# Optimization experiments

Hardware: AMD Instinct MI355X
Metric: run time of the kernel (lower is better)

## Reference

```python
import jax, jax.numpy as jnp
import numpy as np

B, T, E, H = 32, 256, 512, 512


def setup_inputs() -> dict:
    key = jax.random.key(0)
    ks = jax.random.split(key, 9)
    s_e = 1.0 / np.sqrt(E)  # nn.Linear default init bound
    s_h = 1.0 / np.sqrt(H)

    def u(k, shape, s):
        return jax.random.uniform(k, shape, jnp.float32, -s, s)

    # Gate order along the 4H axis: [in, forget, cell, out]
    return {
        "x": jax.random.normal(ks[0], (B, T, E), jnp.float32),
        "fwd_Wih": u(ks[1], (E, 4 * H), s_e),
        "fwd_bih": u(ks[2], (4 * H,), s_e),
        "fwd_Whh": u(ks[3], (H, 4 * H), s_h),
        "fwd_bhh": u(ks[4], (4 * H,), s_h),
        "bwd_Wih": u(ks[5], (E, 4 * H), s_e),
        "bwd_bih": u(ks[6], (4 * H,), s_e),
        "bwd_Whh": u(ks[7], (H, 4 * H), s_h),
        "bwd_bhh": u(ks[8], (4 * H,), s_h),
    }


def _lstm(x_seq, Wih, bih, Whh, bhh):
    """Run one LSTM direction over x_seq [B,T,E]; returns hidden states [B,T,H]
    in scan order (no flipping), matching the torch loop."""
    b, h = x_seq.shape[0], Whh.shape[0]
    # Precompute all input projections (and fold both biases) in one big GEMM.
    xg = jnp.einsum("bte,eg->tbg", x_seq, Wih) + bih + bhh  # [T,B,4H]
    h0 = jnp.zeros((b, h), x_seq.dtype)
    c0 = jnp.zeros((b, h), x_seq.dtype)

    def step(carry, xg_t):
        hprev, cprev = carry
        g = xg_t + hprev @ Whh  # [B,4H]
        i, f, gc, o = jnp.split(g, 4, axis=-1)
        c = jax.nn.sigmoid(f) * cprev + jax.nn.sigmoid(i) * jnp.tanh(gc)
        hnew = jax.nn.sigmoid(o) * jnp.tanh(c)
        return (hnew, c), hnew

    _, hs = jax.lax.scan(step, (h0, c0), xg)  # hs: [T,B,H]
    return hs.transpose(1, 0, 2)


def reference(x, fwd_Wih, fwd_bih, fwd_Whh, fwd_bhh,
              bwd_Wih, bwd_bih, bwd_Whh, bwd_bhh):
    fwd = _lstm(x, fwd_Wih, fwd_bih, fwd_Whh, fwd_bhh)
    # Backward direction processes reversed inputs; outputs are stacked in
    # processing order (the torch module does NOT re-flip them).
    bwd = _lstm(x[:, ::-1, :], bwd_Wih, bwd_bih, bwd_Whh, bwd_bhh)
    return jnp.concatenate([fwd, bwd], axis=-1)  # [B,T,2H]
```

## Files before the change

kernel.cpp:

```cpp
#include <hip/hip_runtime.h>
#include <hip/hip_bf16.h>
#include <math.h>

static constexpr int BB = 32;
static constexpr int TT = 256;
static constexpr int EE = 512;
static constexpr int HH = 512;
static constexpr int GG = 2048;

static constexpr int WS = 20;
static constexpr int HS = 36;

using u16 = unsigned short;

__device__ __forceinline__ float bf2f(u16 u) {
    return __uint_as_float(((unsigned int)u) << 16);
}
__device__ __forceinline__ u16 f2bf(float f) {
    unsigned int u = __float_as_uint(f);
    unsigned int r = 0x7FFFu + ((u >> 16) & 1u);
    return (u16)((u + r) >> 16);
}
__device__ __forceinline__ float sigm(float x) {
    return 1.0f / (1.0f + expf(-x));
}

__device__ __forceinline__ float4 ld_b128_sc(const float4* p) {
    float4 v;
    asm volatile("global_load_dwordx4 %0, %1, off sc0 sc1" : "=v"(v) : "v"(p));
    return v;
}
__device__ __forceinline__ void st_b32_sc(float* p, float v) {
    asm volatile("global_store_dword %0, %1, off sc0 sc1" :: "v"(p), "v"(v) : "memory");
}

template<bool F32>
__device__ __forceinline__ float ldw(const void* p, size_t i) {
    if constexpr (F32) return ((const float*)p)[i];
    else               return bf2f(((const u16*)p)[i]);
}
template<bool F32>
__device__ __forceinline__ float4 ld4(const void* p, size_t i) {
    if constexpr (F32) {
        return *(const float4*)((const float*)p + i);
    } else {
        ushort4 v = *(const ushort4*)((const u16*)p + i);
        return make_float4(bf2f(v.x), bf2f(v.y), bf2f(v.z), bf2f(v.w));
    }
}

__global__ void init_state(const u16* __restrict__ bih_probe,
                           float* __restrict__ h_st, float* __restrict__ c_st,
                           int* __restrict__ bar, int* __restrict__ flag) {
    size_t i = (size_t)blockIdx.x * blockDim.x + threadIdx.x;
    size_t stride = (size_t)gridDim.x * blockDim.x;
    for (size_t j = i; j < (size_t)2*2*BB*HH; j += stride) h_st[j] = 0.0f;
    for (size_t j = i; j < (size_t)2*BB*HH;   j += stride) c_st[j] = 0.0f;
    for (size_t j = i; j < 1024;              j += stride) bar[j] = 0;
    if (blockIdx.x == 0 && threadIdx.x == 0) {
        int f = 0;
        for (int k = 0; k < 2048; ++k) {
            int e = (bih_probe[k] >> 7) & 0xFF;
            if (e >= 127) f = 1;
        }
        *flag = f;
    }
}

template<bool F32>
__device__ __forceinline__ void xg_body(
    const void* __restrict__ x, const void* __restrict__ Wih,
    const void* __restrict__ bih, const void* __restrict__ bhh,
    float* __restrict__ xgp, int d, int mt, int nt, float* b_lds)
{
    const int tid = threadIdx.x;
    const int tn = tid & 15;
    const int tm = tid >> 4;
    const int m0 = mt * 64;
    const int n0 = nt * 64;

    size_t a_off[4];
    #pragma unroll
    for (int i = 0; i < 4; ++i) {
        const int m = m0 + 4*tm + i;
        const int t = m >> 5, b = m & 31;
        const int t_src = d ? (TT - 1 - t) : t;
        a_off[i] = ((size_t)b * TT + t_src) * EE;
    }

    float acc[4][4];
    #pragma unroll
    for (int i = 0; i < 4; ++i)
        #pragma unroll
        for (int j = 0; j < 4; ++j) acc[i][j] = 0.0f;

    const int kr = tid >> 2;
    const int nc = (tid & 3) * 16;

    for (int k0 = 0; k0 < EE; k0 += 64) {
        __syncthreads();
        #pragma unroll 4
        for (int e = 0; e < 16; ++e)
            b_lds[kr*64 + nc + e] = ldw<F32>(Wih, (size_t)(k0 + kr)*GG + n0 + nc + e);
        __syncthreads();

        #pragma unroll 2
        for (int kk = 0; kk < 64; kk += 4) {
            float4 av[4];
            #pragma unroll
            for (int i = 0; i < 4; ++i) av[i] = ld4<F32>(x, a_off[i] + k0 + kk);
            #pragma unroll
            for (int j = 0; j < 4; ++j) {
                const float4 bv = *(const float4*)&b_lds[(kk + j)*64 + 4*tn];
                #pragma unroll
                for (int i = 0; i < 4; ++i) {
                    const float a = (j == 0) ? av[i].x : (j == 1) ? av[i].y
                                  : (j == 2) ? av[i].z : av[i].w;
                    acc[i][0] += a * bv.x; acc[i][1] += a * bv.y;
                    acc[i][2] += a * bv.z; acc[i][3] += a * bv.w;
                }
            }
        }
    }

    const int mbase = m0 + 4*tm;
    const int tt = mbase >> 5, bb = mbase & 31;
    #pragma unroll
    for (int j = 0; j < 4; ++j) {
        const int col  = n0 + 4*tn + j;
        const float bs = ldw<F32>(bih, col) + ldw<F32>(bhh, col);
        const int g    = col >> 9;
        const int nblk = (col & 511) >> 2;
        const int nl   = col & 3;
        const size_t idx = (((size_t)d*TT + tt)*65536)
                         + (size_t)nblk*512 + (size_t)(g*4 + nl)*32 + bb;
        float4 v = make_float4(acc[0][j] + bs, acc[1][j] + bs,
                               acc[2][j] + bs, acc[3][j] + bs);
        *(float4*)&xgp[idx] = v;
    }
}

__global__ __launch_bounds__(256) void xg_gemm(
    const void* __restrict__ x,
    const void* __restrict__ WihF, const void* __restrict__ bihF, const void* __restrict__ bhhF,
    const void* __restrict__ WihB, const void* __restrict__ bihB, const void* __restrict__ bhhB,
    float* __restrict__ xgp, const int* __restrict__ flag)
{
    __shared__ float b_lds[64 * 64];
    const int bid = blockIdx.x;
    const int d  = bid >> 12;
    const int r  = bid & 4095;
    const int mt = r >> 5;
    const int nt = r & 31;
    const void* Wih = d ? WihB : WihF;
    const void* bih = d ? bihB : bihF;
    const void* bhh = d ? bhhB : bhhF;
    if (*flag) xg_body<true >(x, Wih, bih, bhh, xgp, d, mt, nt, b_lds);
    else       xg_body<false>(x, Wih, bih, bhh, xgp, d, mt, nt, b_lds);
}

__device__ __forceinline__ void grid_bar_dir(int* __restrict__ bard, int wgl, int target) {
    asm volatile("s_waitcnt vmcnt(0)" ::: "memory");
    __syncthreads();
    if (threadIdx.x == 0) {
        int v = __hip_atomic_fetch_add(&bard[32 + (wgl >> 4) * 32], 1,
                                       __ATOMIC_RELAXED, __HIP_MEMORY_SCOPE_AGENT);
        if ((v & 15) == 15)
            __hip_atomic_fetch_add(&bard[0], 1, __ATOMIC_RELAXED, __HIP_MEMORY_SCOPE_AGENT);
        while (__hip_atomic_load(&bard[0], __ATOMIC_RELAXED, __HIP_MEMORY_SCOPE_AGENT) < target)
            __builtin_amdgcn_s_sleep(1);
    }
    __syncthreads();
}

template<bool F32>
__device__ __forceinline__ void rec_body(
    const void* __restrict__ Whh,
    const float* __restrict__ xgp,
    float* __restrict__ hT,
    int* __restrict__ bar,
    void* __restrict__ out, int d, int nblk, int wgl,
    float* __restrict__ wT_lds,
    float* __restrict__ h_lds,
    float* __restrict__ gbuf)
{
    const int tid = threadIdx.x;
    const int cg = tid >> 6;
    const int bg = (tid >> 3) & 7;
    const int kg = tid & 7;

    {
        const int ci = tid & 15;
        const int cw = (ci >> 2)*512 + nblk*4 + (ci & 3);
        const int kb = (tid >> 4) * 32;
        #pragma unroll 4
        for (int k = kb; k < kb + 32; ++k)
            wT_lds[k*WS + ci] = ldw<F32>(Whh, (size_t)k*GG + cw);
    }

    int* bard = bar + d*512;
    float cr = 0.0f;
    const int gnl = tid >> 5;
    const int gb  = tid & 31;

    __syncthreads();

    for (int t = 0; t < TT; ++t) {
        const int parity = t & 1;
        const float4* hprev4 = (const float4*)(hT + (size_t)(d*2 + (parity ^ 1)) * 16384);
        float*        hnext  = hT + (size_t)(d*2 + parity) * 16384;

        float xgv[4] = {0.f, 0.f, 0.f, 0.f};
        if (tid < 128) {
            const float* xgs = xgp + (((size_t)d*TT + t)*65536) + (size_t)nblk*512;
            #pragma unroll
            for (int g = 0; g < 4; ++g)
                xgv[g] = xgs[(g*4 + gnl)*32 + gb];
        }

        float4 hstg[16];
        #pragma unroll
        for (int i = 0; i < 16; ++i)
            hstg[i] = ld_b128_sc(hprev4 + i*256 + tid);
        asm volatile("s_waitcnt vmcnt(0)" ::: "memory");
        __builtin_amdgcn_sched_barrier(0);
        #pragma unroll
        for (int i = 0; i < 16; ++i) {
            const int idx = i*256 + tid;
            const int k  = idx >> 3;
            const int b4 = idx & 7;
            *(float4*)&h_lds[k*HS + b4*4] = hstg[i];
        }
        __syncthreads();

        float acc[4][4];
        #pragma unroll
        for (int i = 0; i < 4; ++i)
            #pragma unroll
            for (int j = 0; j < 4; ++j) acc[i][j] = 0.0f;
        {
            const float* wp = wT_lds + kg*WS + cg*4;
            const float* hp = h_lds  + kg*HS + bg*4;
            #pragma unroll 8
            for (int kk = 0; kk < 64; ++kk) {
                const float4 wv = *(const float4*)(wp + kk*(8*WS));
                const float4 hv = *(const float4*)(hp + kk*(8*HS));
                acc[0][0] += wv.x*hv.x; acc[0][1] += wv.x*hv.y; acc[0][2] += wv.x*hv.z; acc[0][3] += wv.x*hv.w;
                acc[1][0] += wv.y*hv.x; acc[1][1] += wv.y*hv.y; acc[1][2] += wv.y*hv.z; acc[1][3] += wv.y*hv.w;
                acc[2][0] += wv.z*hv.x; acc[2][1] += wv.z*hv.y; acc[2][2] += wv.z*hv.z; acc[2][3] += wv.z*hv.w;
                acc[3][0] += wv.w*hv.x; acc[3][1] += wv.w*hv.y; acc[3][2] += wv.w*hv.z; acc[3][3] += wv.w*hv.w;
            }
        }
        #pragma unroll
        for (int i = 0; i < 4; ++i)
            #pragma unroll
            for (int j = 0; j < 4; ++j) {
                float v = acc[i][j];
                v += __shfl_xor(v, 1);
                v += __shfl_xor(v, 2);
                v += __shfl_xor(v, 4);
                acc[i][j] = v;
            }
        if (kg < 4) {
            const int ci = kg;
            *(float4*)&gbuf[(cg*4 + ci)*32 + bg*4] =
                make_float4(acc[ci][0], acc[ci][1], acc[ci][2], acc[ci][3]);
        }
        __syncthreads();

        if (tid < 128) {
            const int nl = gnl;
            const int b  = gb;
            const float gi = gbuf[(0*4 + nl)*32 + b] + xgv[0];
            const float gf = gbuf[(1*4 + nl)*32 + b] + xgv[1];
            const float gc = gbuf[(2*4 + nl)*32 + b] + xgv[2];
            const float go = gbuf[(3*4 + nl)*32 + b] + xgv[3];
            const float cn = sigm(gf)*cr + sigm(gi)*tanhf(gc);
            cr = cn;
            const float hv = sigm(go)*tanhf(cn);
            const int ng = nblk*4 + nl;
            st_b32_sc(hnext + (size_t)ng*32 + b, hv);
            const size_t oi = ((size_t)b*TT + t)*(2*HH) + (size_t)d*HH + ng;
            if constexpr (F32) ((float*)out)[oi] = hv;
            else               ((u16*)out)[oi]   = f2bf(hv);
        }
        grid_bar_dir(bard, wgl, 8 * (t + 1));
    }
}

__global__ __launch_bounds__(256, 1) void lstm_rec(
    const void* __restrict__ WhhF, const void* __restrict__ WhhB,
    const float* __restrict__ xgp, float* __restrict__ hT,
    int* __restrict__ bar, const int* __restrict__ flag,
    void* __restrict__ out)
{
    __shared__ float wT_lds[512 * WS];
    __shared__ float h_lds[512 * HS];
    __shared__ float gbuf[512];
    const int wg   = blockIdx.x;
    const int d    = wg >> 7;
    const int nblk = wg & 127;
    const void* Whh = d ? WhhB : WhhF;
    if (*flag) rec_body<true >(Whh, xgp, hT, bar, out, d, nblk, wg & 127, wT_lds, h_lds, gbuf);
    else       rec_body<false>(Whh, xgp, hT, bar, out, d, nblk, wg & 127, wT_lds, h_lds, gbuf);
}

template<bool F32>
__device__ __forceinline__ void step_body(
    const void* __restrict__ x,
    const void* __restrict__ Wih, const void* __restrict__ bih,
    const void* __restrict__ Whh, const void* __restrict__ bhh,
    const float* __restrict__ h_prev, float* __restrict__ h_next,
    float* __restrict__ c_st, void* __restrict__ out,
    int d, int nblk, int t, int t_src, float* __restrict__ gbuf)
{
    const int tid = threadIdx.x;
    const int c0  = tid & 15;
    const int g   = c0 >> 2;
    const int nl  = c0 & 3;
    const int bq  = tid >> 4;
    const int col = g*512 + nblk*4 + nl;
    const int b0 = bq*2, b1 = b0 + 1;

    float p00=0.f,p01=0.f,p02=0.f,p03=0.f;
    float p10=0.f,p11=0.f,p12=0.f,p13=0.f;
    {
        const size_t xo0 = ((size_t)b0*TT + t_src) * EE;
        const size_t xo1 = ((size_t)b1*TT + t_src) * EE;
        #pragma unroll 4
        for (int k = 0; k < EE; k += 4) {
            const size_t wi = (size_t)k*GG + col;
            float w0 = ldw<F32>(Wih, wi);
            float w1 = ldw<F32>(Wih, wi +   (size_t)GG);
            float w2 = ldw<F32>(Wih, wi + 2*(size_t)GG);
            float w3 = ldw<F32>(Wih, wi + 3*(size_t)GG);
            float4 a0 = ld4<F32>(x, xo0 + k);
            float4 a1 = ld4<F32>(x, xo1 + k);
            p00 += w0*a0.x; p01 += w1*a0.y; p02 += w2*a0.z; p03 += w3*a0.w;
            p10 += w0*a1.x; p11 += w1*a1.y; p12 += w2*a1.z; p13 += w3*a1.w;
        }
    }
    {
        const float* hr0 = h_prev + (size_t)b0*HH;
        const float* hr1 = h_prev + (size_t)b1*HH;
        #pragma unroll 4
        for (int k = 0; k < HH; k += 4) {
            const size_t wi = (size_t)k*GG + col;
            float w0 = ldw<F32>(Whh, wi);
            float w1 = ldw<F32>(Whh, wi +   (size_t)GG);
            float w2 = ldw<F32>(Whh, wi + 2*(size_t)GG);
            float w3 = ldw<F32>(Whh, wi + 3*(size_t)GG);
            float4 v0 = *(const float4*)(hr0 + k);
            float4 v1 = *(const float4*)(hr1 + k);
            p00 += w0*v0.x; p01 += w1*v0.y; p02 += w2*v0.z; p03 += w3*v0.w;
            p10 += w0*v1.x; p11 += w1*v1.y; p12 += w2*v1.z; p13 += w3*v1.w;
        }
    }
    const float bias = ldw<F32>(bih, col) + ldw<F32>(bhh, col);
    gbuf[tid*2 + 0] = p00 + p01 + p02 + p03 + bias;
    gbuf[tid*2 + 1] = p10 + p11 + p12 + p13 + bias;
    __syncthreads();
    if (c0 < 4) {
        const int nlc = c0;
        const int ng  = nblk*4 + nlc;
        #pragma unroll
        for (int bi = 0; bi < 2; ++bi) {
            const int b = bq*2 + bi;
            const float gi = gbuf[(bq*16 + 0  + nlc)*2 + bi];
            const float gf = gbuf[(bq*16 + 4  + nlc)*2 + bi];
            const float gc = gbuf[(bq*16 + 8  + nlc)*2 + bi];
            const float go = gbuf[(bq*16 + 12 + nlc)*2 + bi];
            const size_t ci = (size_t)b*HH + ng;
            const float cp = c_st[ci];
            const float cn = sigm(gf)*cp + sigm(gi)*tanhf(gc);
            c_st[ci] = cn;
            const float hv = sigm(go)*tanhf(cn);
            h_next[ci] = hv;
            const size_t oi = ((size_t)b*TT + t)*(2*HH) + (size_t)d*HH + ng;
            if constexpr (F32) ((float*)out)[oi] = hv;
            else               ((u16*)out)[oi]   = f2bf(hv);
        }
    }
}

__global__ __launch_bounds__(256) void lstm_step(
    const void* __restrict__ x,
    const void* __restrict__ WihF, const void* __restrict__ bihF,
    const void* __restrict__ WhhF, const void* __restrict__ bhhF,
    const void* __restrict__ WihB, const void* __restrict__ bihB,
    const void* __restrict__ WhhB, const void* __restrict__ bhhB,
    float* __restrict__ h_buf, float* __restrict__ c_buf,
    const int* __restrict__ flag, void* __restrict__ out, int t)
{
    __shared__ float gbuf[512];
    const int bid  = blockIdx.x;
    const int d    = bid >> 7;
    const int nblk = bid & 127;
    const void* Wih = d ? WihB : WihF;
    const void* Whh = d ? WhhB : WhhF;
    const void* bih = d ? bihB : bihF;
    const void* bhh = d ? bhhB : bhhF;
    const int t_src  = d ? (TT - 1 - t) : t;
    const int parity = t & 1;
    const float* h_prev = h_buf + ((size_t)(d*2 + (parity ^ 1))) * BB * HH;
    float*       h_next = h_buf + ((size_t)(d*2 + parity)) * BB * HH;
    float*       c_st   = c_buf + (size_t)d * BB * HH;
    if (*flag) step_body<true >(x, Wih, bih, Whh, bhh, h_prev, h_next, c_st, out, d, nblk, t, t_src, gbuf);
    else       step_body<false>(x, Wih, bih, Whh, bhh, h_prev, h_next, c_st, out, d, nblk, t, t_src, gbuf);
}

extern "C" void kernel_launch(void* const* d_in, const int* in_sizes, int n_in,
                              void* d_out, int out_size, void* d_ws, size_t ws_size,
                              hipStream_t stream) {
    const void* x    = d_in[0];
    const void* WihF = d_in[1];
    const void* bihF = d_in[2];
    const void* WhhF = d_in[3];
    const void* bhhF = d_in[4];
    const void* WihB = d_in[5];
    const void* bihB = d_in[6];
    const void* WhhB = d_in[7];
    const void* bhhB = d_in[8];

    float* ws = (float*)d_ws;

    const size_t off_xg = 0;
    const size_t off_h  = (size_t)2*TT*BB*GG;
    const size_t off_c  = off_h + (size_t)2*2*BB*HH;
    const size_t off_b  = off_c + (size_t)2*BB*HH;
    const size_t off_f  = off_b + 1024;
    const size_t need_bytes = (off_f + 16) * sizeof(float);

    if (ws_size >= need_bytes) {
        float* xgp  = ws + off_xg;
        float* hT   = ws + off_h;
        float* cbuf = ws + off_c;
        int*   bar  = (int*)(ws + off_b);
        int*   flag = (int*)(ws + off_f);

        init_state<<<64, 256, 0, stream>>>((const u16*)bihF, hT, cbuf, bar, flag);
        xg_gemm<<<8192, 256, 0, stream>>>(x, WihF, bihF, bhhF, WihB, bihB, bhhB, xgp, flag);
        lstm_rec<<<256, 256, 0, stream>>>(WhhF, WhhB, xgp, hT, bar, flag, d_out);
    } else {
        float* h_buf = ws;
        float* c_buf = ws + (size_t)2*2*BB*HH;
        int*   bar   = (int*)(c_buf + (size_t)2*BB*HH);
        int*   flag  = (int*)(bar + 1024);
        init_state<<<64, 256, 0, stream>>>((const u16*)bihF, h_buf, c_buf, bar, flag);
        for (int t = 0; t < TT; ++t) {
            lstm_step<<<256, 256, 0, stream>>>(x, WihF, bihF, WhhF, bhhF,
                                               WihB, bihB, WhhB, bhhB,
                                               h_buf, c_buf, flag, d_out, t);
        }
    }
}
```

Baseline: 2.629 ms.

## Replace two-level grid barrier with split arrive/wait and chunked h staging

```diff
diff --git a/kernel.cpp b/kernel.cpp
--- a/kernel.cpp
+++ b/kernel.cpp
@@ -32,6 +32,19 @@
 }
 __device__ __forceinline__ void st_b32_sc(float* p, float v) {
     asm volatile("global_store_dword %0, %1, off sc0 sc1" :: "v"(p), "v"(v) : "memory");
+}
+
+__device__ __forceinline__ void waitcnt_chunk(int g) {
+    switch (g) {
+    case 0: asm volatile("s_waitcnt vmcnt(14)" ::: "memory"); break;
+    case 1: asm volatile("s_waitcnt vmcnt(12)" ::: "memory"); break;
+    case 2: asm volatile("s_waitcnt vmcnt(10)" ::: "memory"); break;
+    case 3: asm volatile("s_waitcnt vmcnt(8)"  ::: "memory"); break;
+    case 4: asm volatile("s_waitcnt vmcnt(6)"  ::: "memory"); break;
+    case 5: asm volatile("s_waitcnt vmcnt(4)"  ::: "memory"); break;
+    case 6: asm volatile("s_waitcnt vmcnt(2)"  ::: "memory"); break;
+    default: asm volatile("s_waitcnt vmcnt(0)" ::: "memory"); break;
+    }
 }
 
 template<bool F32>
@@ -159,20 +172,6 @@
     else       xg_body<false>(x, Wih, bih, bhh, xgp, d, mt, nt, b_lds);
 }
 
-__device__ __forceinline__ void grid_bar_dir(int* __restrict__ bard, int wgl, int target) {
-    asm volatile("s_waitcnt vmcnt(0)" ::: "memory");
-    __syncthreads();
-    if (threadIdx.x == 0) {
-        int v = __hip_atomic_fetch_add(&bard[32 + (wgl >> 4) * 32], 1,
-                                       __ATOMIC_RELAXED, __HIP_MEMORY_SCOPE_AGENT);
-        if ((v & 15) == 15)
-            __hip_atomic_fetch_add(&bard[0], 1, __ATOMIC_RELAXED, __HIP_MEMORY_SCOPE_AGENT);
-        while (__hip_atomic_load(&bard[0], __ATOMIC_RELAXED, __HIP_MEMORY_SCOPE_AGENT) < target)
-            __builtin_amdgcn_s_sleep(1);
-    }
-    __syncthreads();
-}
-
 template<bool F32>
 __device__ __forceinline__ void rec_body(
     const void* __restrict__ Whh,
@@ -184,7 +183,8 @@
     float* __restrict__ h_lds,
     float* __restrict__ gbuf)
 {
-    const int tid = threadIdx.x;
+    const int tid  = threadIdx.x;
+    const int lane = tid & 63;
     const int cg = tid >> 6;
     const int bg = (tid >> 3) & 7;
     const int kg = tid & 7;
@@ -199,9 +199,14 @@
     }
 
     int* bard = bar + d*512;
+    int* grpc = bard + 32;
+    const int mygrp = wgl >> 4;
     float cr = 0.0f;
     const int gnl = tid >> 5;
     const int gb  = tid & 31;
+
+    const float* wp = wT_lds + kg*WS + cg*4;
+    const float* hp = h_lds  + kg*HS + bg*4;
 
     __syncthreads();
 
@@ -218,31 +223,44 @@
                 xgv[g] = xgs[(g*4 + gnl)*32 + gb];
         }
 
+        if (t > 0) {
+            const int tgt = 16 * t;
+            while (true) {
+                int v = 0x7fffffff;
+                if (lane < 8)
+                    v = __hip_atomic_load(&grpc[lane*32], __ATOMIC_RELAXED,
+                                          __HIP_MEMORY_SCOPE_AGENT);
+                if (__all(v >= tgt)) break;
+                __builtin_amdgcn_s_sleep(1);
+            }
+        }
+        __builtin_amdgcn_sched_barrier(0);
+
         float4 hstg[16];
         #pragma unroll
         for (int i = 0; i < 16; ++i)
             hstg[i] = ld_b128_sc(hprev4 + i*256 + tid);
-        asm volatile("s_waitcnt vmcnt(0)" ::: "memory");
-        __builtin_amdgcn_sched_barrier(0);
-        #pragma unroll
-        for (int i = 0; i < 16; ++i) {
-            const int idx = i*256 + tid;
-            const int k  = idx >> 3;
-            const int b4 = idx & 7;
-            *(float4*)&h_lds[k*HS + b4*4] = hstg[i];
-        }
-        __syncthreads();
 
         float acc[4][4];
         #pragma unroll
         for (int i = 0; i < 4; ++i)
             #pragma unroll
             for (int j = 0; j < 4; ++j) acc[i][j] = 0.0f;
-        {
-            const float* wp = wT_lds + kg*WS + cg*4;
-            const float* hp = h_lds  + kg*HS + bg*4;
-            #pragma unroll 8
-            for (int kk = 0; kk < 64; ++kk) {
+
+        #pragma unroll
+        for (int g2 = 0; g2 < 8; ++g2) {
+            waitcnt_chunk(g2);
+            #pragma unroll
+            for (int j = 0; j < 2; ++j) {
+                const int idx = (2*g2 + j)*256 + tid;
+                const int k  = idx >> 3;
+                const int b4 = idx & 7;
+                *(float4*)&h_lds[k*HS + b4*4] = hstg[2*g2 + j];
+            }
+            asm volatile("s_waitcnt lgkmcnt(0)\n\ts_barrier" ::: "memory");
+            #pragma unroll
+            for (int kkl = 0; kkl < 8; ++kkl) {
+                const int kk = g2*8 + kkl;
                 const float4 wv = *(const float4*)(wp + kk*(8*WS));
                 const float4 hv = *(const float4*)(hp + kk*(8*HS));
                 acc[0][0] += wv.x*hv.x; acc[0][1] += wv.x*hv.y; acc[0][2] += wv.x*hv.z; acc[0][3] += wv.x*hv.w;
@@ -251,6 +269,7 @@
                 acc[3][0] += wv.w*hv.x; acc[3][1] += wv.w*hv.y; acc[3][2] += wv.w*hv.z; acc[3][3] += wv.w*hv.w;
             }
         }
+
         #pragma unroll
         for (int i = 0; i < 4; ++i)
             #pragma unroll
@@ -284,7 +303,12 @@
             if constexpr (F32) ((float*)out)[oi] = hv;
             else               ((u16*)out)[oi]   = f2bf(hv);
         }
-        grid_bar_dir(bard, wgl, 8 * (t + 1));
+
+        asm volatile("s_waitcnt vmcnt(0)" ::: "memory");
+        __syncthreads();
+        if (tid == 0)
+            __hip_atomic_fetch_add(&grpc[mygrp*32], 1,
+                                   __ATOMIC_RELAXED, __HIP_MEMORY_SCOPE_AGENT);
     }
 }
 
```

Result: slower. 2.852 ms (+8.5%).

## Replace two-level grid barrier with per-group counters and prefetch next-step gate inputs

Applied to the files above, without the earlier changes.

```diff
diff --git a/kernel.cpp b/kernel.cpp
--- a/kernel.cpp
+++ b/kernel.cpp
@@ -25,11 +25,6 @@
     return 1.0f / (1.0f + expf(-x));
 }
 
-__device__ __forceinline__ float4 ld_b128_sc(const float4* p) {
-    float4 v;
-    asm volatile("global_load_dwordx4 %0, %1, off sc0 sc1" : "=v"(v) : "v"(p));
-    return v;
-}
 __device__ __forceinline__ void st_b32_sc(float* p, float v) {
     asm volatile("global_store_dword %0, %1, off sc0 sc1" :: "v"(p), "v"(v) : "memory");
 }
@@ -159,20 +154,6 @@
     else       xg_body<false>(x, Wih, bih, bhh, xgp, d, mt, nt, b_lds);
 }
 
-__device__ __forceinline__ void grid_bar_dir(int* __restrict__ bard, int wgl, int target) {
-    asm volatile("s_waitcnt vmcnt(0)" ::: "memory");
-    __syncthreads();
-    if (threadIdx.x == 0) {
-        int v = __hip_atomic_fetch_add(&bard[32 + (wgl >> 4) * 32], 1,
-                                       __ATOMIC_RELAXED, __HIP_MEMORY_SCOPE_AGENT);
-        if ((v & 15) == 15)
-            __hip_atomic_fetch_add(&bard[0], 1, __ATOMIC_RELAXED, __HIP_MEMORY_SCOPE_AGENT);
-        while (__hip_atomic_load(&bard[0], __ATOMIC_RELAXED, __HIP_MEMORY_SCOPE_AGENT) < target)
-            __builtin_amdgcn_s_sleep(1);
-    }
-    __syncthreads();
-}
-
 template<bool F32>
 __device__ __forceinline__ void rec_body(
     const void* __restrict__ Whh,
@@ -184,7 +165,8 @@
     float* __restrict__ h_lds,
     float* __restrict__ gbuf)
 {
-    const int tid = threadIdx.x;
+    const int tid  = threadIdx.x;
+    const int lane = tid & 63;
     const int cg = tid >> 6;
     const int bg = (tid >> 3) & 7;
     const int kg = tid & 7;
@@ -199,31 +181,51 @@
     }
 
     int* bard = bar + d*512;
+    int* grpc = bard + 32;
+    const int mygrp = wgl >> 4;
     float cr = 0.0f;
     const int gnl = tid >> 5;
     const int gb  = tid & 31;
 
+    const float* wp = wT_lds + kg*WS + cg*4;
+    const float* hp = h_lds  + kg*HS + bg*4;
+
     __syncthreads();
+
+    float xgv[4] = {0.f, 0.f, 0.f, 0.f};
+    if (tid < 128) {
+        const float* xgs = xgp + ((size_t)d*TT)*65536 + (size_t)nblk*512;
+        #pragma unroll
+        for (int g = 0; g < 4; ++g)
+            xgv[g] = xgs[(g*4 + gnl)*32 + gb];
+    }
 
     for (int t = 0; t < TT; ++t) {
         const int parity = t & 1;
         const float4* hprev4 = (const float4*)(hT + (size_t)(d*2 + (parity ^ 1)) * 16384);
         float*        hnext  = hT + (size_t)(d*2 + parity) * 16384;
 
-        float xgv[4] = {0.f, 0.f, 0.f, 0.f};
-        if (tid < 128) {
-            const float* xgs = xgp + (((size_t)d*TT + t)*65536) + (size_t)nblk*512;
-            #pragma unroll
-            for (int g = 0; g < 4; ++g)
-                xgv[g] = xgs[(g*4 + gnl)*32 + gb];
-        }
+        if (tid < 64) {
+            if (t > 0) {
+                const int tgt = 16 * t;
+                while (true) {
+                    int v = 0x7fffffff;
+                    if (lane < 8)
+                        v = __hip_atomic_load(&grpc[lane*32], __ATOMIC_RELAXED,
+                                              __HIP_MEMORY_SCOPE_AGENT);
+                    if (__all(v >= tgt)) break;
+                    __builtin_amdgcn_s_sleep(1);
+                }
+            }
+            __builtin_amdgcn_fence(__ATOMIC_ACQUIRE, "agent");
+            asm volatile("s_waitcnt vmcnt(0)" ::: "memory");
+        }
+        __syncthreads();
 
         float4 hstg[16];
         #pragma unroll
         for (int i = 0; i < 16; ++i)
-            hstg[i] = ld_b128_sc(hprev4 + i*256 + tid);
-        asm volatile("s_waitcnt vmcnt(0)" ::: "memory");
-        __builtin_amdgcn_sched_barrier(0);
+            hstg[i] = hprev4[i*256 + tid];
         #pragma unroll
         for (int i = 0; i < 16; ++i) {
             const int idx = i*256 + tid;
@@ -238,19 +240,16 @@
         for (int i = 0; i < 4; ++i)
             #pragma unroll
             for (int j = 0; j < 4; ++j) acc[i][j] = 0.0f;
-        {
-            const float* wp = wT_lds + kg*WS + cg*4;
-            const float* hp = h_lds  + kg*HS + bg*4;
-            #pragma unroll 8
-            for (int kk = 0; kk < 64; ++kk) {
-                const float4 wv = *(const float4*)(wp + kk*(8*WS));
-                const float4 hv = *(const float4*)(hp + kk*(8*HS));
-                acc[0][0] += wv.x*hv.x; acc[0][1] += wv.x*hv.y; acc[0][2] += wv.x*hv.z; acc[0][3] += wv.x*hv.w;
-                acc[1][0] += wv.y*hv.x; acc[1][1] += wv.y*hv.y; acc[1][2] += wv.y*hv.z; acc[1][3] += wv.y*hv.w;
-                acc[2][0] += wv.z*hv.x; acc[2][1] += wv.z*hv.y; acc[2][2] += wv.z*hv.z; acc[2][3] += wv.z*hv.w;
-                acc[3][0] += wv.w*hv.x; acc[3][1] += wv.w*hv.y; acc[3][2] += wv.w*hv.z; acc[3][3] += wv.w*hv.w;
-            }
-        }
+        #pragma unroll 8
+        for (int kk = 0; kk < 64; ++kk) {
+            const float4 wv = *(const float4*)(wp + kk*(8*WS));
+            const float4 hv = *(const float4*)(hp + kk*(8*HS));
+            acc[0][0] += wv.x*hv.x; acc[0][1] += wv.x*hv.y; acc[0][2] += wv.x*hv.z; acc[0][3] += wv.x*hv.w;
+            acc[1][0] += wv.y*hv.x; acc[1][1] += wv.y*hv.y; acc[1][2] += wv.y*hv.z; acc[1][3] += wv.y*hv.w;
+            acc[2][0] += wv.z*hv.x; acc[2][1] += wv.z*hv.y; acc[2][2] += wv.z*hv.z; acc[2][3] += wv.z*hv.w;
+            acc[3][0] += wv.w*hv.x; acc[3][1] += wv.w*hv.y; acc[3][2] += wv.w*hv.z; acc[3][3] += wv.w*hv.w;
+        }
+
         #pragma unroll
         for (int i = 0; i < 4; ++i)
             #pragma unroll
@@ -283,8 +282,17 @@
             const size_t oi = ((size_t)b*TT + t)*(2*HH) + (size_t)d*HH + ng;
             if constexpr (F32) ((float*)out)[oi] = hv;
             else               ((u16*)out)[oi]   = f2bf(hv);
-        }
-        grid_bar_dir(bard, wgl, 8 * (t + 1));
+            const float* xgs = xgp + (((size_t)d*TT + (t+1))*65536) + (size_t)nblk*512;
+            #pragma unroll
+            for (int g = 0; g < 4; ++g)
+                xgv[g] = xgs[(g*4 + gnl)*32 + gb];
+        }
+
+        asm volatile("s_waitcnt vmcnt(4)" ::: "memory");
+        __syncthreads();
+        if (tid == 0)
+            __hip_atomic_fetch_add(&grpc[mygrp*32], 1,
+                                   __ATOMIC_RELAXED, __HIP_MEMORY_SCOPE_AGENT);
     }
 }
 
```

After: 3.029 ms. +15.2%, slower.
